# Kernel optimization log

Hardware: AMD Instinct MI355X
Metric: run time of the kernel (lower is better)

The kernel has to match this reference:

```python
import jax, jax.numpy as jnp
import numpy as np

N = 8192
D = 128
NUM_CLASSES = 100
EPS = 1e-8  # torch CosineSimilarity default eps


def _l2_normalize(x):
    # torch cosine sim divides by max(||x||, eps)
    n = jnp.sqrt(jnp.sum(x * x, axis=-1, keepdims=True))
    return x / jnp.maximum(n, EPS)


def _remove_diag(M):
    # [n, n] -> [n, n-1], dropping the diagonal, no boolean gather needed
    n = M.shape[0]
    return M.reshape(-1)[1:].reshape(n - 1, n + 1)[:, :-1].reshape(n, n - 1)


def setup_inputs() -> dict:
    key = jax.random.key(0)
    k1, k2, k3, k4 = jax.random.split(key, 4)
    inst_embed = jax.random.normal(k1, (N, D), dtype=jnp.float32)
    proxy = jax.random.normal(k2, (N, D), dtype=jnp.float32)
    negative_mask = jax.random.randint(k3, (NUM_CLASSES, N), 0, 2).astype(jnp.float32)
    labels = jax.random.randint(k4, (N,), 0, NUM_CLASSES, dtype=jnp.int64) if jax.config.jax_enable_x64 else jax.random.randint(k4, (N,), 0, NUM_CLASSES, dtype=jnp.int32)
    return {
        "inst_embed": inst_embed,
        "proxy": proxy,
        "negative_mask": negative_mask,
        "labels": labels,
        "temperature": jnp.float32(0.07),
        "margin": jnp.float32(0.0),
    }


def reference(inst_embed, proxy, negative_mask, labels, temperature, margin):
    xn = _l2_normalize(inst_embed)                       # [N, D]
    # pairwise cosine similarity via normalize + matmul (not NxNxD broadcast)
    sim = xn @ xn.T                                      # [N, N]
    instance_zone = jnp.exp((_remove_diag(sim) - margin) / temperature)  # [N, N-1]

    pn = _l2_normalize(proxy)
    inst2proxy_positive = jnp.exp((jnp.sum(xn * pn, axis=-1) - margin) / temperature)  # [N]

    # pos_collected_numerator == True branch
    mask = _remove_diag(negative_mask[labels])           # [N, N-1]
    numerator = jnp.sum(instance_zone * mask, axis=1) + inst2proxy_positive
    denominator = inst2proxy_positive + jnp.sum(instance_zone, axis=1)
    return -jnp.mean(jnp.log(numerator / denominator))
```

## Files before the change

kernel.cpp:

```cpp
#include <hip/hip_runtime.h>
#include <stdint.h>

#define NROWS 8192
#define DD 128
#define EPS 1e-8f
#define LOG2E 1.4426950408889634f

#define SPLIT 16
#define RPB 128
#define CPT 32
#define LDS_COL 272
#define NORM_BLOCKS (NROWS / 4)
#define PACK_BLOCKS 3200

typedef __bf16 bf16x8 __attribute__((ext_vector_type(8)));
typedef float f32x4 __attribute__((ext_vector_type(4)));

__device__ __forceinline__ unsigned int f2bf(float f) {
  union { float f; unsigned int u; } v; v.f = f;
  unsigned int u = v.u;
  return (u + 0x7fffu + ((u >> 16) & 1u)) >> 16;
}
__device__ __forceinline__ float bf2f(unsigned int b) {
  union { unsigned int u; float f; } v; v.u = b << 16;
  return v.f;
}

__global__ __launch_bounds__(256) void norm_kernel(
    const float* __restrict__ x, const float* __restrict__ pr,
    const float* __restrict__ nm, const int* __restrict__ lb,
    const float* __restrict__ tptr,
    unsigned short* __restrict__ xnA, unsigned short* __restrict__ xnB,
    float* __restrict__ p, float* __restrict__ eself, float* __restrict__ mii,
    float* __restrict__ tot, float* __restrict__ msk,
    unsigned int* __restrict__ packed, float* __restrict__ out)
{
  int wave = threadIdx.x >> 6, lane = threadIdx.x & 63;
  int bx = blockIdx.x;

  if (bx >= NORM_BLOCKS) {
    int widx = (bx - NORM_BLOCKS) * 4 + wave;
    int cls = widx >> 7;
    int w64 = widx & 127;
    float v = nm[(size_t)cls * NROWS + w64 * 64 + lane];
    unsigned long long b = __ballot(v != 0.0f);
    if (lane == 0) {
      packed[cls * 256 + w64 * 2] = (unsigned int)b;
      packed[cls * 256 + w64 * 2 + 1] = (unsigned int)(b >> 32);
    }
    return;
  }

  int row = bx * 4 + wave;
  float2 xv = ((const float2*)(x + (size_t)row * DD))[lane];
  float2 pv = ((const float2*)(pr + (size_t)row * DD))[lane];
  float sx = xv.x * xv.x + xv.y * xv.y;
  float sp = pv.x * pv.x + pv.y * pv.y;
  float dp = xv.x * pv.x + xv.y * pv.y;
  #pragma unroll
  for (int m = 1; m < 64; m <<= 1) {
    sx += __shfl_xor(sx, m);
    sp += __shfl_xor(sp, m);
    dp += __shfl_xor(dp, m);
  }
  float inx = 1.f / fmaxf(sqrtf(sx), EPS);
  float inp = 1.f / fmaxf(sqrtf(sp), EPS);
  float s1 = LOG2E / tptr[0];

  unsigned int a0 = f2bf(xv.x * inx * s1), a1 = f2bf(xv.y * inx * s1);
  unsigned int b0 = f2bf(xv.x * inx),      b1 = f2bf(xv.y * inx);
  ((unsigned int*)(xnA + (size_t)row * DD))[lane] = a0 | (a1 << 16);
  ((unsigned int*)(xnB + (size_t)row * DD))[lane] = b0 | (b1 << 16);

  float ss = bf2f(a0) * bf2f(b0) + bf2f(a1) * bf2f(b1);
  #pragma unroll
  for (int m = 1; m < 64; m <<= 1) ss += __shfl_xor(ss, m);

  if (lane == 0) {
    p[row] = __builtin_amdgcn_exp2f(dp * inx * inp * s1);
    eself[row] = __builtin_amdgcn_exp2f(ss);
    mii[row] = nm[(size_t)lb[row] * NROWS + row];
    tot[row] = 0.f;
    msk[row] = 0.f;
    if (row == 0) out[0] = 0.f;
  }
}

__global__ __launch_bounds__(256, 4) void main_kernel(
    const unsigned short* __restrict__ xnA_u, const unsigned short* __restrict__ xnB_u,
    const unsigned int* __restrict__ packed, const int* __restrict__ labels,
    float* __restrict__ tot, float* __restrict__ msk)
{
  __shared__ unsigned char lds[CPT * LDS_COL];
  int tid = threadIdx.x;
  int wave = tid >> 6, lane = tid & 63;
  int q = lane >> 4, c = lane & 15;
  int rb0 = blockIdx.x * RPB + wave * 16;
  int rb1 = rb0 + 64;

  const bf16x8* xnvA = (const bf16x8*)xnA_u;

  bf16x8 a0[4], a1[4];
  {
    const bf16x8* b = xnvA + (size_t)(rb0 + c) * (DD / 8) + q;
    a0[0] = b[0]; a0[1] = b[4]; a0[2] = b[8]; a0[3] = b[12];
  }
  {
    const bf16x8* b = xnvA + (size_t)(rb1 + c) * (DD / 8) + q;
    a1[0] = b[0]; a1[1] = b[4]; a1[2] = b[8]; a1[3] = b[12];
  }

  int jb = blockIdx.y * (NROWS / SPLIT);
  const int NT = (NROWS / SPLIT) / CPT;

  int r0[4], r1[4];
  unsigned int offP0[4], offP1[4];
  #pragma unroll
  for (int k = 0; k < 4; k++) {
    r0[k] = rb0 + q * 4 + k;
    r1[k] = rb1 + q * 4 + k;
    offP0[k] = (unsigned int)labels[r0[k]] * 256u + (unsigned int)(jb >> 5);
    offP1[k] = (unsigned int)labels[r1[k]] * 256u + (unsigned int)(jb >> 5);
  }
  float t0[4] = {0, 0, 0, 0}, m0[4] = {0, 0, 0, 0};
  float t1[4] = {0, 0, 0, 0}, m1[4] = {0, 0, 0, 0};

  int scol = tid >> 4, schunk = tid & 15;
  uint4* ldsw0 = (uint4*)(lds + scol * LDS_COL + schunk * 16);
  uint4* ldsw1 = (uint4*)(lds + (scol + 16) * LDS_COL + schunk * 16);
  const char* gB = (const char*)xnB_u;
  const char* gbase0 = gB + (size_t)(jb + scol) * 256 + schunk * 16;
  const char* gbase1 = gbase0 + 16 * 256;

  uint4 g0 = *(const uint4*)(gbase0);
  uint4 g1 = *(const uint4*)(gbase1);
  unsigned int wn0[4], wn1[4];
  #pragma unroll
  for (int k = 0; k < 4; k++) {
    wn0[k] = packed[offP0[k]];
    wn1[k] = packed[offP1[k]];
  }

  for (int t = 0; t < NT; t++) {
    __syncthreads();
    *ldsw0 = g0;
    *ldsw1 = g1;
    unsigned int wc0[4], wc1[4];
    #pragma unroll
    for (int k = 0; k < 4; k++) { wc0[k] = wn0[k]; wc1[k] = wn1[k]; }

    int tn = (t + 1 < NT) ? t + 1 : 0;
    g0 = *(const uint4*)(gbase0 + (size_t)tn * (CPT * 256));
    g1 = *(const uint4*)(gbase1 + (size_t)tn * (CPT * 256));
    #pragma unroll
    for (int k = 0; k < 4; k++) {
      wn0[k] = packed[offP0[k] + tn];
      wn1[k] = packed[offP1[k] + tn];
    }
    __syncthreads();

    #pragma unroll
    for (int s = 0; s < 2; s++) {
      const bf16x8* bl = (const bf16x8*)(lds + (unsigned)(s * 16 + c) * LDS_COL + q * 16);
      bf16x8 b0 = bl[0], b1 = bl[4], b2 = bl[8], b3 = bl[12];

      f32x4 acc0 = {0, 0, 0, 0};
      f32x4 acc1 = {0, 0, 0, 0};
      acc0 = __builtin_amdgcn_mfma_f32_16x16x32_bf16(a0[0], b0, acc0, 0, 0, 0);
      acc1 = __builtin_amdgcn_mfma_f32_16x16x32_bf16(a1[0], b0, acc1, 0, 0, 0);
      acc0 = __builtin_amdgcn_mfma_f32_16x16x32_bf16(a0[1], b1, acc0, 0, 0, 0);
      acc1 = __builtin_amdgcn_mfma_f32_16x16x32_bf16(a1[1], b1, acc1, 0, 0, 0);
      acc0 = __builtin_amdgcn_mfma_f32_16x16x32_bf16(a0[2], b2, acc0, 0, 0, 0);
      acc1 = __builtin_amdgcn_mfma_f32_16x16x32_bf16(a1[2], b2, acc1, 0, 0, 0);
      acc0 = __builtin_amdgcn_mfma_f32_16x16x32_bf16(a0[3], b3, acc0, 0, 0, 0);
      acc1 = __builtin_amdgcn_mfma_f32_16x16x32_bf16(a1[3], b3, acc1, 0, 0, 0);

      int pos = s * 16 + c;
      #pragma unroll
      for (int k = 0; k < 4; k++) {
        float e = __builtin_amdgcn_exp2f(acc0[k]);
        t0[k] += e;
        m0[k] = fmaf(e, (float)((wc0[k] >> pos) & 1u), m0[k]);
      }
      #pragma unroll
      for (int k = 0; k < 4; k++) {
        float e = __builtin_amdgcn_exp2f(acc1[k]);
        t1[k] += e;
        m1[k] = fmaf(e, (float)((wc1[k] >> pos) & 1u), m1[k]);
      }
    }
  }

  #pragma unroll
  for (int sh = 1; sh < 16; sh <<= 1) {
    #pragma unroll
    for (int k = 0; k < 4; k++) {
      t0[k] += __shfl_xor(t0[k], sh);
      m0[k] += __shfl_xor(m0[k], sh);
      t1[k] += __shfl_xor(t1[k], sh);
      m1[k] += __shfl_xor(m1[k], sh);
    }
  }
  if (c == 0) {
    #pragma unroll
    for (int k = 0; k < 4; k++) {
      atomicAdd(&tot[r0[k]], t0[k]);
      atomicAdd(&msk[r0[k]], m0[k]);
      atomicAdd(&tot[r1[k]], t1[k]);
      atomicAdd(&msk[r1[k]], m1[k]);
    }
  }
}

__global__ __launch_bounds__(256) void loss_kernel(
    const float* __restrict__ p, const float* __restrict__ tot,
    const float* __restrict__ msk, const float* __restrict__ eself,
    const float* __restrict__ mii, float* __restrict__ out)
{
  __shared__ float sd[4];
  int r = blockIdx.x * 256 + threadIdx.x;
  float pi = p[r];
  float es = eself[r];
  float t = tot[r] - es;
  float m = msk[r] - es * mii[r];
  float v = __builtin_amdgcn_logf(pi + t) - __builtin_amdgcn_logf(pi + m);
  float s = v * (1.0f / (LOG2E * (float)NROWS));
  #pragma unroll
  for (int sh = 1; sh < 64; sh <<= 1) s += __shfl_xor(s, sh);
  int wave = threadIdx.x >> 6, lane = threadIdx.x & 63;
  if (lane == 0) sd[wave] = s;
  __syncthreads();
  if (threadIdx.x == 0) atomicAdd(out, sd[0] + sd[1] + sd[2] + sd[3]);
}

extern "C" void kernel_launch(void* const* d_in, const int* in_sizes, int n_in,
                              void* d_out, int out_size, void* d_ws, size_t ws_size,
                              hipStream_t stream) {
  const float* x  = (const float*)d_in[0];
  const float* pr = (const float*)d_in[1];
  const float* nm = (const float*)d_in[2];
  const int*   lb = (const int*)d_in[3];
  const float* tp = (const float*)d_in[4];

  char* ws = (char*)d_ws;
  unsigned short* xnA = (unsigned short*)ws;
  unsigned short* xnB = xnA + (size_t)NROWS * DD;
  float* p     = (float*)(xnB + (size_t)NROWS * DD);
  float* tot   = p + NROWS;
  float* msk   = tot + NROWS;
  float* eself = msk + NROWS;
  float* miiv  = eself + NROWS;
  unsigned int* packed = (unsigned int*)(miiv + NROWS);
  float* out = (float*)d_out;

  norm_kernel<<<NORM_BLOCKS + PACK_BLOCKS, 256, 0, stream>>>(
      x, pr, nm, lb, tp, xnA, xnB, p, eself, miiv, tot, msk, packed, out);
  main_kernel<<<dim3(NROWS / RPB, SPLIT), 256, 0, stream>>>(xnA, xnB, packed,
                                                            lb, tot, msk);
  loss_kernel<<<NROWS / 256, 256, 0, stream>>>(p, tot, msk, eself, miiv, out);
}
```

Measured before the change: 103.4 us.

## Double-buffer LDS column tiles and double columns per iteration

Doubles the column tile per iteration from 32 to 64 and adds a second LDS buffer, so each iteration writes the next tile into the other buffer and needs one barrier instead of two. The mask words are now loaded as 64-bit pairs inside the iteration rather than prefetched a step ahead. This cuts barrier count and loop overhead in exchange for double the LDS footprint, about 34 KB per block, which may reduce how many blocks fit per CU, and the mask loads are now exposed latency.

Result: slower. 133.1 us (+28.7%).

```diff
diff --git a/kernel.cpp b/kernel.cpp
--- a/kernel.cpp
+++ b/kernel.cpp
@@ -8,8 +8,9 @@
 
 #define SPLIT 16
 #define RPB 128
-#define CPT 32
+#define CPT 64
 #define LDS_COL 272
+#define NT ((NROWS / SPLIT) / CPT)
 #define NORM_BLOCKS (NROWS / 4)
 #define PACK_BLOCKS 3200
 
@@ -91,7 +92,7 @@
     const unsigned int* __restrict__ packed, const int* __restrict__ labels,
     float* __restrict__ tot, float* __restrict__ msk)
 {
-  __shared__ unsigned char lds[CPT * LDS_COL];
+  __shared__ unsigned char lds[2][CPT * LDS_COL];
   int tid = threadIdx.x;
   int wave = tid >> 6, lane = tid & 63;
   int q = lane >> 4, c = lane & 15;
@@ -111,7 +112,6 @@
   }
 
   int jb = blockIdx.y * (NROWS / SPLIT);
-  const int NT = (NROWS / SPLIT) / CPT;
 
   int r0[4], r1[4];
   unsigned int offP0[4], offP1[4];
@@ -126,42 +126,41 @@
   float t1[4] = {0, 0, 0, 0}, m1[4] = {0, 0, 0, 0};
 
   int scol = tid >> 4, schunk = tid & 15;
-  uint4* ldsw0 = (uint4*)(lds + scol * LDS_COL + schunk * 16);
-  uint4* ldsw1 = (uint4*)(lds + (scol + 16) * LDS_COL + schunk * 16);
   const char* gB = (const char*)xnB_u;
-  const char* gbase0 = gB + (size_t)(jb + scol) * 256 + schunk * 16;
-  const char* gbase1 = gbase0 + 16 * 256;
-
-  uint4 g0 = *(const uint4*)(gbase0);
-  uint4 g1 = *(const uint4*)(gbase1);
-  unsigned int wn0[4], wn1[4];
-  #pragma unroll
-  for (int k = 0; k < 4; k++) {
-    wn0[k] = packed[offP0[k]];
-    wn1[k] = packed[offP1[k]];
-  }
+  const char* gbase = gB + (size_t)(jb + scol) * 256 + schunk * 16;
+  unsigned int ldsoff = (unsigned int)(scol * LDS_COL + schunk * 16);
+
+  uint4 g0, g1, g2, g3;
+  g0 = *(const uint4*)(gbase);
+  g1 = *(const uint4*)(gbase + 16 * 256);
+  g2 = *(const uint4*)(gbase + 32 * 256);
+  g3 = *(const uint4*)(gbase + 48 * 256);
+  *(uint4*)(lds[0] + ldsoff)                 = g0;
+  *(uint4*)(lds[0] + ldsoff + 16 * LDS_COL)  = g1;
+  *(uint4*)(lds[0] + ldsoff + 32 * LDS_COL)  = g2;
+  *(uint4*)(lds[0] + ldsoff + 48 * LDS_COL)  = g3;
+  __syncthreads();
 
   for (int t = 0; t < NT; t++) {
-    __syncthreads();
-    *ldsw0 = g0;
-    *ldsw1 = g1;
-    unsigned int wc0[4], wc1[4];
-    #pragma unroll
-    for (int k = 0; k < 4; k++) { wc0[k] = wn0[k]; wc1[k] = wn1[k]; }
-
-    int tn = (t + 1 < NT) ? t + 1 : 0;
-    g0 = *(const uint4*)(gbase0 + (size_t)tn * (CPT * 256));
-    g1 = *(const uint4*)(gbase1 + (size_t)tn * (CPT * 256));
+    uint2 wc0[4], wc1[4];
     #pragma unroll
     for (int k = 0; k < 4; k++) {
-      wn0[k] = packed[offP0[k] + tn];
-      wn1[k] = packed[offP1[k] + tn];
-    }
-    __syncthreads();
-
-    #pragma unroll
-    for (int s = 0; s < 2; s++) {
-      const bf16x8* bl = (const bf16x8*)(lds + (unsigned)(s * 16 + c) * LDS_COL + q * 16);
+      wc0[k] = *(const uint2*)&packed[offP0[k] + 2 * t];
+      wc1[k] = *(const uint2*)&packed[offP1[k] + 2 * t];
+    }
+
+    if (t + 1 < NT) {
+      const char* gb = gbase + (size_t)(t + 1) * (CPT * 256);
+      g0 = *(const uint4*)(gb);
+      g1 = *(const uint4*)(gb + 16 * 256);
+      g2 = *(const uint4*)(gb + 32 * 256);
+      g3 = *(const uint4*)(gb + 48 * 256);
+    }
+
+    const unsigned char* buf = lds[t & 1];
+    #pragma unroll
+    for (int s = 0; s < 4; s++) {
+      const bf16x8* bl = (const bf16x8*)(buf + (unsigned)(s * 16 + c) * LDS_COL + q * 16);
       bf16x8 b0 = bl[0], b1 = bl[4], b2 = bl[8], b3 = bl[12];
 
       f32x4 acc0 = {0, 0, 0, 0};
@@ -175,20 +174,31 @@
       acc0 = __builtin_amdgcn_mfma_f32_16x16x32_bf16(a0[3], b3, acc0, 0, 0, 0);
       acc1 = __builtin_amdgcn_mfma_f32_16x16x32_bf16(a1[3], b3, acc1, 0, 0, 0);
 
-      int pos = s * 16 + c;
+      int sh = s * 16 + c;
       #pragma unroll
       for (int k = 0; k < 4; k++) {
+        unsigned int w = (sh & 32) ? wc0[k].y : wc0[k].x;
         float e = __builtin_amdgcn_exp2f(acc0[k]);
         t0[k] += e;
-        m0[k] = fmaf(e, (float)((wc0[k] >> pos) & 1u), m0[k]);
+        m0[k] = fmaf(e, (float)((w >> (sh & 31)) & 1u), m0[k]);
       }
       #pragma unroll
       for (int k = 0; k < 4; k++) {
+        unsigned int w = (sh & 32) ? wc1[k].y : wc1[k].x;
         float e = __builtin_amdgcn_exp2f(acc1[k]);
         t1[k] += e;
-        m1[k] = fmaf(e, (float)((wc1[k] >> pos) & 1u), m1[k]);
+        m1[k] = fmaf(e, (float)((w >> (sh & 31)) & 1u), m1[k]);
       }
     }
+
+    if (t + 1 < NT) {
+      unsigned char* nb = (unsigned char*)lds[(t + 1) & 1];
+      *(uint4*)(nb + ldsoff)                 = g0;
+      *(uint4*)(nb + ldsoff + 16 * LDS_COL)  = g1;
+      *(uint4*)(nb + ldsoff + 32 * LDS_COL)  = g2;
+      *(uint4*)(nb + ldsoff + 48 * LDS_COL)  = g3;
+    }
+    __syncthreads();
   }
 
   #pragma unroll
```

## Pre-swizzle B operand into MFMA fragment layout and drop LDS staging

Applied to the files above, without the earlier changes.

The norm kernel now writes the normalized B matrix in a tiled layout that matches the MFMA B-fragment order per 16-column group. The main kernel then loads B fragments straight from global memory into registers with a one-step register prefetch. This removes the shared-memory tile, both __syncthreads per iteration and the LDS reads and writes. In exchange, every wave in a block reloads the same B data from global/L2 instead of sharing it, and the packed mask words are now loaded inside the loop rather than prefetched.

Result: slower. 109.9 us (+6.3%).

```diff
diff --git a/kernel.cpp b/kernel.cpp
--- a/kernel.cpp
+++ b/kernel.cpp
@@ -8,8 +8,7 @@
 
 #define SPLIT 16
 #define RPB 128
-#define CPT 32
-#define LDS_COL 272
+#define NSUB ((NROWS / SPLIT) / 16)
 #define NORM_BLOCKS (NROWS / 4)
 #define PACK_BLOCKS 3200
 
@@ -25,12 +24,15 @@
   union { unsigned int u; float f; } v; v.u = b << 16;
   return v.f;
 }
+__device__ __forceinline__ bf16x8 u2b(uint4 u) {
+  union { uint4 u; bf16x8 b; } v; v.u = u; return v.b;
+}
 
 __global__ __launch_bounds__(256) void norm_kernel(
     const float* __restrict__ x, const float* __restrict__ pr,
     const float* __restrict__ nm, const int* __restrict__ lb,
     const float* __restrict__ tptr,
-    unsigned short* __restrict__ xnA, unsigned short* __restrict__ xnB,
+    unsigned short* __restrict__ xnA, unsigned char* __restrict__ xnBt,
     float* __restrict__ p, float* __restrict__ eself, float* __restrict__ mii,
     float* __restrict__ tot, float* __restrict__ msk,
     unsigned int* __restrict__ packed, float* __restrict__ out)
@@ -70,7 +72,13 @@
   unsigned int a0 = f2bf(xv.x * inx * s1), a1 = f2bf(xv.y * inx * s1);
   unsigned int b0 = f2bf(xv.x * inx),      b1 = f2bf(xv.y * inx);
   ((unsigned int*)(xnA + (size_t)row * DD))[lane] = a0 | (a1 << 16);
-  ((unsigned int*)(xnB + (size_t)row * DD))[lane] = b0 | (b1 << 16);
+
+  {
+    int kstep = lane >> 4, qq = (lane >> 2) & 3, pos = lane & 3;
+    unsigned int dst = ((unsigned int)(row >> 4)) * 4096u + kstep * 1024u +
+                       qq * 256u + (row & 15) * 16u + pos * 4u;
+    *(unsigned int*)(xnBt + dst) = b0 | (b1 << 16);
+  }
 
   float ss = bf2f(a0) * bf2f(b0) + bf2f(a1) * bf2f(b1);
   #pragma unroll
@@ -87,11 +95,10 @@
 }
 
 __global__ __launch_bounds__(256, 4) void main_kernel(
-    const unsigned short* __restrict__ xnA_u, const unsigned short* __restrict__ xnB_u,
+    const unsigned short* __restrict__ xnA_u, const unsigned char* __restrict__ xnBt,
     const unsigned int* __restrict__ packed, const int* __restrict__ labels,
     float* __restrict__ tot, float* __restrict__ msk)
 {
-  __shared__ unsigned char lds[CPT * LDS_COL];
   int tid = threadIdx.x;
   int wave = tid >> 6, lane = tid & 63;
   int q = lane >> 4, c = lane & 15;
@@ -111,7 +118,6 @@
   }
 
   int jb = blockIdx.y * (NROWS / SPLIT);
-  const int NT = (NROWS / SPLIT) / CPT;
 
   int r0[4], r1[4];
   unsigned int offP0[4], offP1[4];
@@ -125,69 +131,56 @@
   float t0[4] = {0, 0, 0, 0}, m0[4] = {0, 0, 0, 0};
   float t1[4] = {0, 0, 0, 0}, m1[4] = {0, 0, 0, 0};
 
-  int scol = tid >> 4, schunk = tid & 15;
-  uint4* ldsw0 = (uint4*)(lds + scol * LDS_COL + schunk * 16);
-  uint4* ldsw1 = (uint4*)(lds + (scol + 16) * LDS_COL + schunk * 16);
-  const char* gB = (const char*)xnB_u;
-  const char* gbase0 = gB + (size_t)(jb + scol) * 256 + schunk * 16;
-  const char* gbase1 = gbase0 + 16 * 256;
-
-  uint4 g0 = *(const uint4*)(gbase0);
-  uint4 g1 = *(const uint4*)(gbase1);
-  unsigned int wn0[4], wn1[4];
-  #pragma unroll
-  for (int k = 0; k < 4; k++) {
-    wn0[k] = packed[offP0[k]];
-    wn1[k] = packed[offP1[k]];
-  }
-
-  for (int t = 0; t < NT; t++) {
-    __syncthreads();
-    *ldsw0 = g0;
-    *ldsw1 = g1;
+  const unsigned char* gB = xnBt + (size_t)(jb >> 4) * 4096 +
+                            (unsigned int)(q * 256 + c * 16);
+
+  uint4 nb0 = *(const uint4*)(gB);
+  uint4 nb1 = *(const uint4*)(gB + 1024);
+  uint4 nb2 = *(const uint4*)(gB + 2048);
+  uint4 nb3 = *(const uint4*)(gB + 3072);
+
+  for (int t = 0; t < NSUB; t++) {
+    bf16x8 b0 = u2b(nb0), b1 = u2b(nb1), b2 = u2b(nb2), b3 = u2b(nb3);
+
+    if (t + 1 < NSUB) {
+      const unsigned char* gb = gB + (size_t)(t + 1) * 4096;
+      nb0 = *(const uint4*)(gb);
+      nb1 = *(const uint4*)(gb + 1024);
+      nb2 = *(const uint4*)(gb + 2048);
+      nb3 = *(const uint4*)(gb + 3072);
+    }
+
     unsigned int wc0[4], wc1[4];
-    #pragma unroll
-    for (int k = 0; k < 4; k++) { wc0[k] = wn0[k]; wc1[k] = wn1[k]; }
-
-    int tn = (t + 1 < NT) ? t + 1 : 0;
-    g0 = *(const uint4*)(gbase0 + (size_t)tn * (CPT * 256));
-    g1 = *(const uint4*)(gbase1 + (size_t)tn * (CPT * 256));
-    #pragma unroll
-    for (int k = 0; k < 4; k++) {
-      wn0[k] = packed[offP0[k] + tn];
-      wn1[k] = packed[offP1[k] + tn];
-    }
-    __syncthreads();
-
-    #pragma unroll
-    for (int s = 0; s < 2; s++) {
-      const bf16x8* bl = (const bf16x8*)(lds + (unsigned)(s * 16 + c) * LDS_COL + q * 16);
-      bf16x8 b0 = bl[0], b1 = bl[4], b2 = bl[8], b3 = bl[12];
-
-      f32x4 acc0 = {0, 0, 0, 0};
-      f32x4 acc1 = {0, 0, 0, 0};
-      acc0 = __builtin_amdgcn_mfma_f32_16x16x32_bf16(a0[0], b0, acc0, 0, 0, 0);
-      acc1 = __builtin_amdgcn_mfma_f32_16x16x32_bf16(a1[0], b0, acc1, 0, 0, 0);
-      acc0 = __builtin_amdgcn_mfma_f32_16x16x32_bf16(a0[1], b1, acc0, 0, 0, 0);
-      acc1 = __builtin_amdgcn_mfma_f32_16x16x32_bf16(a1[1], b1, acc1, 0, 0, 0);
-      acc0 = __builtin_amdgcn_mfma_f32_16x16x32_bf16(a0[2], b2, acc0, 0, 0, 0);
-      acc1 = __builtin_amdgcn_mfma_f32_16x16x32_bf16(a1[2], b2, acc1, 0, 0, 0);
-      acc0 = __builtin_amdgcn_mfma_f32_16x16x32_bf16(a0[3], b3, acc0, 0, 0, 0);
-      acc1 = __builtin_amdgcn_mfma_f32_16x16x32_bf16(a1[3], b3, acc1, 0, 0, 0);
-
-      int pos = s * 16 + c;
-      #pragma unroll
-      for (int k = 0; k < 4; k++) {
-        float e = __builtin_amdgcn_exp2f(acc0[k]);
-        t0[k] += e;
-        m0[k] = fmaf(e, (float)((wc0[k] >> pos) & 1u), m0[k]);
-      }
-      #pragma unroll
-      for (int k = 0; k < 4; k++) {
-        float e = __builtin_amdgcn_exp2f(acc1[k]);
-        t1[k] += e;
-        m1[k] = fmaf(e, (float)((wc1[k] >> pos) & 1u), m1[k]);
-      }
+    int g = t >> 1;
+    #pragma unroll
+    for (int k = 0; k < 4; k++) {
+      wc0[k] = packed[offP0[k] + g];
+      wc1[k] = packed[offP1[k] + g];
+    }
+
+    f32x4 acc0 = {0, 0, 0, 0};
+    f32x4 acc1 = {0, 0, 0, 0};
+    acc0 = __builtin_amdgcn_mfma_f32_16x16x32_bf16(a0[0], b0, acc0, 0, 0, 0);
+    acc1 = __builtin_amdgcn_mfma_f32_16x16x32_bf16(a1[0], b0, acc1, 0, 0, 0);
+    acc0 = __builtin_amdgcn_mfma_f32_16x16x32_bf16(a0[1], b1, acc0, 0, 0, 0);
+    acc1 = __builtin_amdgcn_mfma_f32_16x16x32_bf16(a1[1], b1, acc1, 0, 0, 0);
+    acc0 = __builtin_amdgcn_mfma_f32_16x16x32_bf16(a0[2], b2, acc0, 0, 0, 0);
+    acc1 = __builtin_amdgcn_mfma_f32_16x16x32_bf16(a1[2], b2, acc1, 0, 0, 0);
+    acc0 = __builtin_amdgcn_mfma_f32_16x16x32_bf16(a0[3], b3, acc0, 0, 0, 0);
+    acc1 = __builtin_amdgcn_mfma_f32_16x16x32_bf16(a1[3], b3, acc1, 0, 0, 0);
+
+    int pos = (t & 1) * 16 + c;
+    #pragma unroll
+    for (int k = 0; k < 4; k++) {
+      float e = __builtin_amdgcn_exp2f(acc0[k]);
+      t0[k] += e;
+      m0[k] = fmaf(e, (float)((wc0[k] >> pos) & 1u), m0[k]);
+    }
+    #pragma unroll
+    for (int k = 0; k < 4; k++) {
+      float e = __builtin_amdgcn_exp2f(acc1[k]);
+      t1[k] += e;
+      m1[k] = fmaf(e, (float)((wc1[k] >> pos) & 1u), m1[k]);
     }
   }
 
@@ -244,8 +237,8 @@
 
   char* ws = (char*)d_ws;
   unsigned short* xnA = (unsigned short*)ws;
-  unsigned short* xnB = xnA + (size_t)NROWS * DD;
-  float* p     = (float*)(xnB + (size_t)NROWS * DD);
+  unsigned char* xnBt = (unsigned char*)(xnA + (size_t)NROWS * DD);
+  float* p     = (float*)(xnBt + (size_t)NROWS * DD * 2);
   float* tot   = p + NROWS;
   float* msk   = tot + NROWS;
   float* eself = msk + NROWS;
@@ -254,8 +247,8 @@
   float* out = (float*)d_out;
 
   norm_kernel<<<NORM_BLOCKS + PACK_BLOCKS, 256, 0, stream>>>(
-      x, pr, nm, lb, tp, xnA, xnB, p, eself, miiv, tot, msk, packed, out);
-  main_kernel<<<dim3(NROWS / RPB, SPLIT), 256, 0, stream>>>(xnA, xnB, packed,
+      x, pr, nm, lb, tp, xnA, xnBt, p, eself, miiv, tot, msk, packed, out);
+  main_kernel<<<dim3(NROWS / RPB, SPLIT), 256, 0, stream>>>(xnA, xnBt, packed,
                                                             lb, tot, msk);
   loss_kernel<<<NROWS / 256, 256, 0, stream>>>(p, tot, msk, eself, miiv, out);
 }
```
